# Performance work log

Measured on AMD Instinct MI355X. Metric: run time of the kernel, lower is better.

The kernel has to match this reference:

```python
import jax, jax.numpy as jnp
import numpy as np

B, N, P = 64, 800000, 128          # batch, total CpG features, n_pathways (capsules)
H1, H2, C = 256, 128, 32           # MLP hidden_topology and n_output
EPS = 1e-5                         # BatchNorm1d eps


def _xavier(key, fan_in, fan_out, shape):
    bound = np.sqrt(6.0 / (fan_in + fan_out))
    return jax.random.uniform(key, shape, jnp.float32, -bound, bound)


def setup_inputs() -> dict:
    key = jax.random.key(0)
    ks = jax.random.split(key, 10)
    x = jax.random.normal(ks[0], (B, N), jnp.float32)
    # idx: sorted pathway assignment, equal capsule sizes N//P (matches module_lens)
    idx = jnp.sort(jax.random.randint(ks[1], (N,), 0, P)).astype(jnp.int64)
    # SPWModulesLayer.weight: xavier_uniform on shape (1, N)
    w = _xavier(ks[2], N, 1, (N,))
    co_w = jax.random.uniform(ks[3], (P,), jnp.float32, 0.0, 4.0)  # CancelOut init
    bn0_g, bn0_b = jnp.ones(P, jnp.float32), jnp.zeros(P, jnp.float32)
    W1, b1 = _xavier(ks[4], P, H1, (P, H1)), jnp.zeros(H1, jnp.float32)
    bn1_g, bn1_b = jnp.ones(H1, jnp.float32), jnp.zeros(H1, jnp.float32)
    W2, b2 = _xavier(ks[5], H1, H2, (H1, H2)), jnp.zeros(H2, jnp.float32)
    bn2_g, bn2_b = jnp.ones(H2, jnp.float32), jnp.zeros(H2, jnp.float32)
    Wo, bo = _xavier(ks[6], H2, C, (H2, C)), jnp.zeros(C, jnp.float32)
    return {"x": x, "w": w, "co_w": co_w,
            "bn0_g": bn0_g, "bn0_b": bn0_b,
            "W1": W1, "b1": b1, "bn1_g": bn1_g, "bn1_b": bn1_b,
            "W2": W2, "b2": b2, "bn2_g": bn2_g, "bn2_b": bn2_b,
            "Wo": Wo, "bo": bo, "idx": idx}


def _bn(z, g, b):
    # BatchNorm1d in training mode: batch mean, biased variance
    m = jnp.mean(z, axis=0)
    v = jnp.mean((z - m) ** 2, axis=0)
    return (z - m) * jax.lax.rsqrt(v + EPS) * g + b


def reference(x, w, co_w, bn0_g, bn0_b, W1, b1, bn1_g, bn1_b,
              W2, b2, bn2_g, bn2_b, Wo, bo, idx):
    # --- SPWModulesLayer: weighted scatter_add over pathway index (last dim) ---
    WX = jnp.zeros((x.shape[0], P), x.dtype).at[:, idx].add(x * w)   # [B, P]
    Z = _bn(jax.nn.relu(WX), bn0_g, bn0_b)                           # ReLU + BN
    Z = Z * jax.nn.sigmoid(co_w)                                     # CancelOut
    # --- MLP head: Linear->ReLU->BN twice, then Linear->Softmax ---
    h = _bn(jax.nn.relu(Z @ W1 + b1), bn1_g, bn1_b)
    h = _bn(jax.nn.relu(h @ W2 + b2), bn2_g, bn2_b)
    y = jax.nn.softmax(h @ Wo + bo, axis=-1)
    return (y, Z)
```

## Files before the change

### kernel.cpp

```cpp
#include <hip/hip_runtime.h>
#include <hip/hip_bf16.h>

#define BB     64
#define NF4    200000
#define CHUNKS 3125
#define NP     128
#define NH1    256
#define NH2    128
#define NC     32
#define EPSV   1e-5f

typedef float fx4 __attribute__((ext_vector_type(4)));

#define AS_G __attribute__((address_space(1)))
#define AS_L __attribute__((address_space(3)))

__device__ __forceinline__ float dot4(fx4 a, fx4 b) {
    return fmaf(a[0], b[0], fmaf(a[1], b[1], fmaf(a[2], b[2], a[3] * b[3])));
}

__global__ __launch_bounds__(64) void k_scatter(
    const float* __restrict__ x, const float* __restrict__ w,
    const int* __restrict__ idx, float* __restrict__ WX)
{
    __shared__ char lds[8 * 1024];
    const int lane = threadIdx.x;
    const int wid  = blockIdx.x;
    const int ch   = wid >> 1;
    const int bh   = (wid & 1) << 5;
    const int n4   = ch * 64 + lane;

    const fx4*  __restrict__ w4 = reinterpret_cast<const fx4*>(w);
    const int4* __restrict__ p4 = reinterpret_cast<const int4*>(idx);
    const fx4*  __restrict__ x4 = reinterpret_cast<const fx4*>(x);

    const fx4  wv = w4[n4];
    const int4 pv = p4[n4];
    const int  pLo = __builtin_amdgcn_readfirstlane(pv.x);
    const int  pHi = __shfl(pv.w, 63);
    const bool uniform = (pLo == pHi);

    fx4 wLo, wHi;
    wLo[0] = (pv.x == pLo) ? wv[0] : 0.f;  wHi[0] = (pv.x == pHi) ? wv[0] : 0.f;
    wLo[1] = (pv.y == pLo) ? wv[1] : 0.f;  wHi[1] = (pv.y == pHi) ? wv[1] : 0.f;
    wLo[2] = (pv.z == pLo) ? wv[2] : 0.f;  wHi[2] = (pv.z == pHi) ? wv[2] : 0.f;
    wLo[3] = (pv.w == pLo) ? wv[3] : 0.f;  wHi[3] = (pv.w == pHi) ? wv[3] : 0.f;

    #pragma unroll
    for (int i = 0; i < 7; ++i) {
        const float* gp = (const float*)(x4 + ((size_t)(bh + i) * NF4 + n4));
        __builtin_amdgcn_global_load_lds((const AS_G float*)gp,
                                         (AS_L float*)(lds + i * 1024), 16, 0, 0);
    }

    #pragma unroll
    for (int i = 0; i < 32; ++i) {
        if (i < 25) {
            asm volatile("s_waitcnt vmcnt(6)" ::: "memory");
        } else if (i == 25) {
            asm volatile("s_waitcnt vmcnt(0)" ::: "memory");
        }
        __builtin_amdgcn_sched_barrier(0);

        const fx4 xr = *reinterpret_cast<const fx4*>(lds + (i & 7) * 1024 + lane * 16);
        float sLo = dot4(xr, wLo);
        if (uniform) {
            #pragma unroll
            for (int off = 1; off < 64; off <<= 1)
                sLo += __shfl_xor(sLo, off);
            if (lane == 0)
                atomicAdd(&WX[(bh + i) * NP + pLo], sLo);
        } else {
            float sHi = dot4(xr, wHi);
            #pragma unroll
            for (int off = 1; off < 64; off <<= 1) {
                sLo += __shfl_xor(sLo, off);
                sHi += __shfl_xor(sHi, off);
            }
            if (lane == 0) {
                atomicAdd(&WX[(bh + i) * NP + pLo], sLo);
                atomicAdd(&WX[(bh + i) * NP + pHi], sHi);
            }
        }
        __builtin_amdgcn_sched_barrier(0);

        if (i < 25) {
            const float* gp = (const float*)(x4 + ((size_t)(bh + i + 7) * NF4 + n4));
            __builtin_amdgcn_global_load_lds((const AS_G float*)gp,
                                             (AS_L float*)(lds + ((i + 7) & 7) * 1024),
                                             16, 0, 0);
        }
        __builtin_amdgcn_sched_barrier(0);
    }
}

__global__ void k_bn0(const float* __restrict__ WX,
                      const float* __restrict__ co_w,
                      const float* __restrict__ g,
                      const float* __restrict__ beta,
                      float* __restrict__ Z)
{
    const int p = threadIdx.x;
    float sum = 0.f, sq = 0.f;
    for (int b = 0; b < BB; ++b) {
        float r = fmaxf(WX[b * NP + p], 0.f);
        sum += r; sq += r * r;
    }
    const float m   = sum * (1.f / BB);
    const float var = sq * (1.f / BB) - m * m;
    const float sc  = rsqrtf(var + EPSV) * g[p];
    const float bt  = beta[p];
    const float sig = 1.f / (1.f + expf(-co_w[p]));
    for (int b = 0; b < BB; ++b) {
        float r = fmaxf(WX[b * NP + p], 0.f);
        Z[b * NP + p] = ((r - m) * sc + bt) * sig;
    }
}

template <int K, int NOUT>
__global__ void k_fc_bn(const float* __restrict__ in,
                        const float* __restrict__ W,
                        const float* __restrict__ bias,
                        const float* __restrict__ g,
                        const float* __restrict__ beta,
                        float* __restrict__ out)
{
    const int j = blockIdx.x;
    const int b = threadIdx.x;
    const float* __restrict__ row = in + b * K;
    float acc = bias[j];
    #pragma unroll 8
    for (int k = 0; k < K; ++k)
        acc = fmaf(row[k], W[k * NOUT + j], acc);
    acc = fmaxf(acc, 0.f);
    float s = acc, q = acc * acc;
    #pragma unroll
    for (int off = 32; off > 0; off >>= 1) {
        s += __shfl_xor(s, off);
        q += __shfl_xor(q, off);
    }
    const float m   = s * (1.f / BB);
    const float var = q * (1.f / BB) - m * m;
    out[b * NOUT + j] = (acc - m) * rsqrtf(var + EPSV) * g[j] + beta[j];
}

__global__ void k_head(const float* __restrict__ h,
                       const float* __restrict__ Wo,
                       const float* __restrict__ bo,
                       float* __restrict__ y)
{
    const int b = blockIdx.x;
    const int c = threadIdx.x;
    const float* __restrict__ row = h + b * NH2;
    float acc = bo[c];
    #pragma unroll 8
    for (int k = 0; k < NH2; ++k)
        acc = fmaf(row[k], Wo[k * NC + c], acc);
    float mx = acc;
    #pragma unroll
    for (int off = 16; off > 0; off >>= 1)
        mx = fmaxf(mx, __shfl_xor(mx, off));
    const float e = expf(acc - mx);
    float s = e;
    #pragma unroll
    for (int off = 16; off > 0; off >>= 1)
        s += __shfl_xor(s, off);
    y[b * NC + c] = e / s;
}

extern "C" void kernel_launch(void* const* d_in, const int* in_sizes, int n_in,
                              void* d_out, int out_size, void* d_ws, size_t ws_size,
                              hipStream_t stream)
{
    const float* x    = (const float*)d_in[0];
    const float* w    = (const float*)d_in[1];
    const float* co_w = (const float*)d_in[2];
    const float* bn0g = (const float*)d_in[3];
    const float* bn0b = (const float*)d_in[4];
    const float* W1   = (const float*)d_in[5];
    const float* b1   = (const float*)d_in[6];
    const float* bn1g = (const float*)d_in[7];
    const float* bn1b = (const float*)d_in[8];
    const float* W2   = (const float*)d_in[9];
    const float* b2   = (const float*)d_in[10];
    const float* bn2g = (const float*)d_in[11];
    const float* bn2b = (const float*)d_in[12];
    const float* Wo   = (const float*)d_in[13];
    const float* bo   = (const float*)d_in[14];
    const int*   idx  = (const int*)d_in[15];

    float* out = (float*)d_out;
    float* y   = out;
    float* Z   = out + BB * NC;

    float* WX = (float*)d_ws;
    float* h1 = WX + BB * NP;
    float* h2 = h1 + BB * NH1;

    hipMemsetAsync(WX, 0, BB * NP * sizeof(float), stream);
    k_scatter<<<CHUNKS * 2, 64, 0, stream>>>(x, w, idx, WX);
    k_bn0<<<1, NP, 0, stream>>>(WX, co_w, bn0g, bn0b, Z);
    k_fc_bn<NP, NH1><<<NH1, BB, 0, stream>>>(Z, W1, b1, bn1g, bn1b, h1);
    k_fc_bn<NH1, NH2><<<NH2, BB, 0, stream>>>(h1, W2, b2, bn2g, bn2b, h2);
    k_head<<<BB, NC, 0, stream>>>(h2, Wo, bo, y);
}
```

Baseline: 89.10 us.

## Fuse BN0 into FC1, transpose hidden layouts, reorder scatter prefetch

Several changes land together. The scatter kernel now issues each next-stage global-to-LDS prefetch before the wait and reads LDS with inline asm, dropping the sched barriers. The single-block BN0 kernel is folded into the first FC layer, which each block recomputes redundantly into LDS. Hidden activations are stored transposed so the per-batch-lane reads coalesce, and the memset is replaced with a small zero kernel. Together these aim to cut launch count and serial tail latency. The risk is that the inline asm waits on lgkmcnt(0) every iteration, and the prefetch is now issued before the wait with the same vmcnt(6), which changes how many loads are in flight.

```diff
diff --git a/kernel.cpp b/kernel.cpp
--- a/kernel.cpp
+++ b/kernel.cpp
@@ -46,23 +46,31 @@
     wLo[2] = (pv.z == pLo) ? wv[2] : 0.f;  wHi[2] = (pv.z == pHi) ? wv[2] : 0.f;
     wLo[3] = (pv.w == pLo) ? wv[3] : 0.f;  wHi[3] = (pv.w == pHi) ? wv[3] : 0.f;
 
-    #pragma unroll
-    for (int i = 0; i < 7; ++i) {
-        const float* gp = (const float*)(x4 + ((size_t)(bh + i) * NF4 + n4));
+    auto stage = [&](int bi) {
+        const float* gp = (const float*)(x4 + ((size_t)(bh + bi) * NF4 + n4));
         __builtin_amdgcn_global_load_lds((const AS_G float*)gp,
-                                         (AS_L float*)(lds + i * 1024), 16, 0, 0);
-    }
+                                         (AS_L float*)(lds + (bi & 7) * 1024),
+                                         16, 0, 0);
+    };
+
+    #pragma unroll
+    for (int i = 0; i < 7; ++i) stage(i);
 
     #pragma unroll
     for (int i = 0; i < 32; ++i) {
         if (i < 25) {
+            stage(i + 7);
             asm volatile("s_waitcnt vmcnt(6)" ::: "memory");
         } else if (i == 25) {
             asm volatile("s_waitcnt vmcnt(0)" ::: "memory");
         }
-        __builtin_amdgcn_sched_barrier(0);
-
-        const fx4 xr = *reinterpret_cast<const fx4*>(lds + (i & 7) * 1024 + lane * 16);
+
+        const unsigned laddr =
+            (unsigned)(size_t)(AS_L char*)(lds + (i & 7) * 1024 + lane * 16);
+        fx4 xr;
+        asm volatile("ds_read_b128 %0, %1\n\ts_waitcnt lgkmcnt(0)"
+                     : "=v"(xr) : "v"(laddr));
+
         float sLo = dot4(xr, wLo);
         if (uniform) {
             #pragma unroll
@@ -82,58 +90,18 @@
                 atomicAdd(&WX[(bh + i) * NP + pHi], sHi);
             }
         }
-        __builtin_amdgcn_sched_barrier(0);
-
-        if (i < 25) {
-            const float* gp = (const float*)(x4 + ((size_t)(bh + i + 7) * NF4 + n4));
-            __builtin_amdgcn_global_load_lds((const AS_G float*)gp,
-                                             (AS_L float*)(lds + ((i + 7) & 7) * 1024),
-                                             16, 0, 0);
-        }
-        __builtin_amdgcn_sched_barrier(0);
     }
 }
 
-__global__ void k_bn0(const float* __restrict__ WX,
-                      const float* __restrict__ co_w,
-                      const float* __restrict__ g,
-                      const float* __restrict__ beta,
-                      float* __restrict__ Z)
-{
-    const int p = threadIdx.x;
-    float sum = 0.f, sq = 0.f;
-    for (int b = 0; b < BB; ++b) {
-        float r = fmaxf(WX[b * NP + p], 0.f);
-        sum += r; sq += r * r;
-    }
-    const float m   = sum * (1.f / BB);
-    const float var = sq * (1.f / BB) - m * m;
-    const float sc  = rsqrtf(var + EPSV) * g[p];
-    const float bt  = beta[p];
-    const float sig = 1.f / (1.f + expf(-co_w[p]));
-    for (int b = 0; b < BB; ++b) {
-        float r = fmaxf(WX[b * NP + p], 0.f);
-        Z[b * NP + p] = ((r - m) * sc + bt) * sig;
-    }
-}
-
-template <int K, int NOUT>
-__global__ void k_fc_bn(const float* __restrict__ in,
-                        const float* __restrict__ W,
-                        const float* __restrict__ bias,
-                        const float* __restrict__ g,
-                        const float* __restrict__ beta,
-                        float* __restrict__ out)
-{
-    const int j = blockIdx.x;
-    const int b = threadIdx.x;
-    const float* __restrict__ row = in + b * K;
-    float acc = bias[j];
-    #pragma unroll 8
-    for (int k = 0; k < K; ++k)
-        acc = fmaf(row[k], W[k * NOUT + j], acc);
-    acc = fmaxf(acc, 0.f);
-    float s = acc, q = acc * acc;
+__global__ void k_zero(float* __restrict__ WX)
+{
+    const int i = blockIdx.x * 256 + threadIdx.x;
+    if (i < BB * NP) WX[i] = 0.f;
+}
+
+__device__ __forceinline__ float bn_shfl(float a, float gj, float bj)
+{
+    float s = a, q = a * a;
     #pragma unroll
     for (int off = 32; off > 0; off >>= 1) {
         s += __shfl_xor(s, off);
@@ -141,21 +109,81 @@
     }
     const float m   = s * (1.f / BB);
     const float var = q * (1.f / BB) - m * m;
-    out[b * NOUT + j] = (acc - m) * rsqrtf(var + EPSV) * g[j] + beta[j];
-}
-
-__global__ void k_head(const float* __restrict__ h,
+    return (a - m) * rsqrtf(var + EPSV) * gj + bj;
+}
+
+__global__ __launch_bounds__(256) void k_fc1z(
+    const float* __restrict__ WX,   const float* __restrict__ co_w,
+    const float* __restrict__ bn0g, const float* __restrict__ bn0b,
+    const float* __restrict__ W1,   const float* __restrict__ b1,
+    const float* __restrict__ bn1g, const float* __restrict__ bn1b,
+    float* __restrict__ Zout, float* __restrict__ h1t)
+{
+    __shared__ float Zl[NP * 65];
+    const int tid  = threadIdx.x;
+    const int wv   = tid >> 6;
+    const int lane = tid & 63;
+    const int blk  = blockIdx.x;
+
+    if (tid < NP) {
+        const int p = tid;
+        float sum = 0.f, sq = 0.f;
+        #pragma unroll 8
+        for (int b = 0; b < BB; ++b) {
+            const float r = fmaxf(WX[b * NP + p], 0.f);
+            sum += r; sq += r * r;
+        }
+        const float m   = sum * (1.f / BB);
+        const float var = sq * (1.f / BB) - m * m;
+        const float sc  = rsqrtf(var + EPSV) * bn0g[p];
+        const float bt  = bn0b[p];
+        const float sig = 1.f / (1.f + expf(-co_w[p]));
+        #pragma unroll 8
+        for (int b = 0; b < BB; ++b) {
+            const float r = fmaxf(WX[b * NP + p], 0.f);
+            const float z = ((r - m) * sc + bt) * sig;
+            Zl[p * 65 + b] = z;
+            if (blk == 0) Zout[b * NP + p] = z;
+        }
+    }
+    __syncthreads();
+
+    const int j = blk * 4 + wv;
+    float acc = b1[j];
+    #pragma unroll 8
+    for (int k = 0; k < NP; ++k)
+        acc = fmaf(Zl[k * 65 + lane], W1[k * NH1 + j], acc);
+    h1t[j * BB + lane] = bn_shfl(fmaxf(acc, 0.f), bn1g[j], bn1b[j]);
+}
+
+template <int K, int NOUT>
+__global__ void k_fc_bn_t(const float* __restrict__ in_t,
+                          const float* __restrict__ W,
+                          const float* __restrict__ bias,
+                          const float* __restrict__ g,
+                          const float* __restrict__ beta,
+                          float* __restrict__ out_t)
+{
+    const int j = blockIdx.x;
+    const int b = threadIdx.x;
+    float acc = bias[j];
+    #pragma unroll 8
+    for (int k = 0; k < K; ++k)
+        acc = fmaf(in_t[k * BB + b], W[k * NOUT + j], acc);
+    out_t[j * BB + b] = bn_shfl(fmaxf(acc, 0.f), g[j], beta[j]);
+}
+
+__global__ void k_head(const float* __restrict__ h2t,
                        const float* __restrict__ Wo,
                        const float* __restrict__ bo,
                        float* __restrict__ y)
 {
     const int b = blockIdx.x;
     const int c = threadIdx.x;
-    const float* __restrict__ row = h + b * NH2;
     float acc = bo[c];
     #pragma unroll 8
     for (int k = 0; k < NH2; ++k)
-        acc = fmaf(row[k], Wo[k * NC + c], acc);
+        acc = fmaf(h2t[k * BB + b], Wo[k * NC + c], acc);
     float mx = acc;
     #pragma unroll
     for (int off = 16; off > 0; off >>= 1)
@@ -193,14 +221,14 @@
     float* y   = out;
     float* Z   = out + BB * NC;
 
-    float* WX = (float*)d_ws;
-    float* h1 = WX + BB * NP;
-    float* h2 = h1 + BB * NH1;
-
-    hipMemsetAsync(WX, 0, BB * NP * sizeof(float), stream);
+    float* WX  = (float*)d_ws;
+    float* h1t = WX + BB * NP;
+    float* h2t = h1t + BB * NH1;
+
+    k_zero<<<32, 256, 0, stream>>>(WX);
     k_scatter<<<CHUNKS * 2, 64, 0, stream>>>(x, w, idx, WX);
-    k_bn0<<<1, NP, 0, stream>>>(WX, co_w, bn0g, bn0b, Z);
-    k_fc_bn<NP, NH1><<<NH1, BB, 0, stream>>>(Z, W1, b1, bn1g, bn1b, h1);
-    k_fc_bn<NH1, NH2><<<NH2, BB, 0, stream>>>(h1, W2, b2, bn2g, bn2b, h2);
-    k_head<<<BB, NC, 0, stream>>>(h2, Wo, bo, y);
-}
+    k_fc1z<<<64, 256, 0, stream>>>(WX, co_w, bn0g, bn0b,
+                                   W1, b1, bn1g, bn1b, Z, h1t);
+    k_fc_bn_t<NH1, NH2><<<NH2, BB, 0, stream>>>(h1t, W2, b2, bn2g, bn2b, h2t);
+    k_head<<<BB, NC, 0, stream>>>(h2t, Wo, bo, y);
+}
```

Measured after the change: 91.85 us. 1.03x slower.
